# Optimization experiments

Hardware: AMD Instinct MI355X
Metric: run time of the kernel (lower is better)

Reference implementation:

```python
import jax, jax.numpy as jnp
import numpy as np

B = 64; SEQ = 512; PRED = 96; D = 321; HID = 2048
WIN = 64; STRIDE = WIN // 2; FT = WIN // 2 + 1
LOW = int(FT * 0.3); MID = int(FT * 0.4); HIGH = FT - LOW - MID  # 9, 13, 11
NW = SEQ // STRIDE + 1; EMBED = NW * WIN  # 17, 1088
EPS = 1e-5; SCALE = 0.02
LH = int(LOW * 2.0); MH = int(MID * 2.0); HH = int(HIGH * 2.0)  # 18, 26, 22


def _clayer(key, fan_in, fan_out):
    k1, k2, k3, k4 = jax.random.split(key, 4)
    return (jax.random.normal(k1, (fan_in, fan_out), jnp.float32) * SCALE,
            jax.random.normal(k2, (fan_in, fan_out), jnp.float32) * SCALE,
            jax.random.normal(k3, (fan_out,), jnp.float32) * SCALE,
            jax.random.normal(k4, (fan_out,), jnp.float32) * SCALE)


def setup_inputs() -> dict:
    key = jax.random.key(0)
    ks = jax.random.split(key, 12)
    inp = {}
    inp["x"] = jax.random.normal(ks[0], (B, SEQ, D), jnp.float32)
    inp["x_mark_enc"] = jax.random.normal(ks[1], (B, SEQ, 4), jnp.float32)
    inp["x_dec"] = jax.random.normal(ks[2], (B, PRED, D), jnp.float32)
    inp["x_mark_dec"] = jax.random.normal(ks[3], (B, PRED, 4), jnp.float32)
    n = jnp.arange(WIN, dtype=jnp.float32)
    inp["window"] = 0.5 * (1.0 - jnp.cos(2.0 * jnp.pi * n / WIN))  # torch.hann_window (periodic)
    inp["revin_w"] = jnp.ones((D,), jnp.float32)
    inp["revin_b"] = jnp.zeros((D,), jnp.float32)
    # low band filter: 3 complex layers LOW->LH->LH->LOW
    for i, (fi, fo) in enumerate([(LOW, LH), (LH, LH), (LH, LOW)]):
        wr, wi, br, bi = _clayer(jax.random.fold_in(ks[4], i), fi, fo)
        inp[f"low{i}_wr"], inp[f"low{i}_wi"], inp[f"low{i}_br"], inp[f"low{i}_bi"] = wr, wi, br, bi
    # mid band filter: 2 complex layers MID->MH->MID
    for i, (fi, fo) in enumerate([(MID, MH), (MH, MID)]):
        wr, wi, br, bi = _clayer(jax.random.fold_in(ks[5], i), fi, fo)
        inp[f"mid{i}_wr"], inp[f"mid{i}_wi"], inp[f"mid{i}_br"], inp[f"mid{i}_bi"] = wr, wi, br, bi
    # high band filter: 1 complex layer HIGH->HIGH
    wr, wi, br, bi = _clayer(ks[6], HIGH, HIGH)
    inp["high0_wr"], inp["high0_wi"], inp["high0_br"], inp["high0_bi"] = wr, wi, br, bi
    inp["fc1_w"] = jax.random.normal(ks[7], (EMBED, HID), jnp.float32) * SCALE
    inp["fc1_b"] = jnp.zeros((HID,), jnp.float32)
    inp["fc2_w"] = jax.random.normal(ks[8], (HID, PRED), jnp.float32) * SCALE
    inp["fc2_b"] = jnp.zeros((PRED,), jnp.float32)
    return inp


def _clin(z, wr, wi, br, bi):
    return z @ (wr + 1j * wi) + (br + 1j * bi)


def _cact(z):
    return jax.nn.leaky_relu(z.real) + 1j * jax.nn.leaky_relu(z.imag)


def reference(x, x_mark_enc, x_dec, x_mark_dec, window, revin_w, revin_b,
              low0_wr, low0_wi, low0_br, low0_bi,
              low1_wr, low1_wi, low1_br, low1_bi,
              low2_wr, low2_wi, low2_br, low2_bi,
              mid0_wr, mid0_wi, mid0_br, mid0_bi,
              mid1_wr, mid1_wi, mid1_br, mid1_bi,
              high0_wr, high0_wi, high0_br, high0_bi,
              fc1_w, fc1_b, fc2_w, fc2_b):
    # RevIN norm over time dim
    mean = jnp.mean(x, axis=1, keepdims=True)
    std = jnp.sqrt(jnp.var(x, axis=1, keepdims=True) + EPS)
    xn = (x - mean) / std * revin_w + revin_b
    xc = jnp.transpose(xn, (0, 2, 1))                      # [B, D, L]
    xp = jnp.pad(xc, ((0, 0), (0, 0), (STRIDE, STRIDE)))
    # batched window extraction (replaces python loop over windows)
    idx = jnp.arange(NW)[:, None] * STRIDE + jnp.arange(WIN)[None, :]
    seg = xp[:, :, idx]
    w = window / jnp.linalg.norm(window)
    xf = jnp.fft.rfft(seg * w, axis=-1)                    # [B, D, NW, FT] complex
    low = xf[..., :LOW]
    mid = xf[..., LOW:LOW + MID]
    high = xf[..., LOW + MID:]
    low = _clin(_cact(_clin(_cact(_clin(low, low0_wr, low0_wi, low0_br, low0_bi)),
                            low1_wr, low1_wi, low1_br, low1_bi)),
                low2_wr, low2_wi, low2_br, low2_bi)
    mid = _clin(_cact(_clin(mid, mid0_wr, mid0_wi, mid0_br, mid0_bi)),
                mid1_wr, mid1_wi, mid1_br, mid1_bi)
    high = _clin(high, high0_wr, high0_wi, high0_br, high0_bi)
    xfil = jnp.concatenate([low, mid, high], axis=-1)      # [B, D, NW, FT]
    xt = jnp.fft.irfft(xfil, n=WIN, axis=-1)
    emb = xt.reshape(x.shape[0], D, EMBED)
    h = jax.nn.leaky_relu(emb @ fc1_w + fc1_b)
    y = h @ fc2_w + fc2_b                                  # [B, D, PRED]
    y = jnp.transpose(y, (0, 2, 1))                        # [B, PRED, D]
    # RevIN denorm
    y = (y - revin_b) / (revin_w + EPS * EPS) * std + mean
    return y
```

## Files before the change

### kernel.cpp

```cpp
#include <hip/hip_runtime.h>

typedef unsigned short u16;
typedef unsigned int   u32;
typedef __attribute__((ext_vector_type(4))) float  fvec4;
typedef __attribute__((ext_vector_type(8))) __bf16 bvec8;

#define NB    64
#define SEQL  512
#define DCH   321
#define BDTOT (NB * DCH)
#define NWIN  17
#define PREDL 96
#define MWTOT (BDTOT * NWIN)
#define KPAD  1152

__device__ __forceinline__ u16 f2bf(float f) {
    union { float f; u32 u; } v; v.f = f;
    u32 r = v.u + 0x7FFFu + ((v.u >> 16) & 1u);
    return (u16)(r >> 16);
}
__device__ __forceinline__ float lrelu(float v) { return v > 0.f ? v : 0.01f * v; }

__device__ __forceinline__ void gld16(const u16* g, u16* l) {
    __builtin_amdgcn_global_load_lds((const __attribute__((address_space(1))) void*)g,
                                     (__attribute__((address_space(3))) void*)l, 16, 0, 0);
}

__global__ __launch_bounds__(256) void stats_kernel(const float* __restrict__ x,
                                                    float* __restrict__ mean,
                                                    float* __restrict__ rstd,
                                                    float* __restrict__ stdv) {
    __shared__ float ls[2][4][64];
    int i = threadIdx.x & 63;
    int j = threadIdx.x >> 6;
    int bd = blockIdx.x * 64 + i;
    int b = bd / DCH, d = bd - b * DCH;
    float s = 0.f, ss = 0.f;
    for (int t = j; t < SEQL; t += 4) {
        float v = x[((size_t)b * SEQL + t) * DCH + d];
        s += v; ss += v * v;
    }
    ls[0][j][i] = s; ls[1][j][i] = ss;
    __syncthreads();
    if (j == 0) {
        s  = ls[0][0][i] + ls[0][1][i] + ls[0][2][i] + ls[0][3][i];
        ss = ls[1][0][i] + ls[1][1][i] + ls[1][2][i] + ls[1][3][i];
        float m   = s * (1.f / SEQL);
        float var = ss * (1.f / SEQL) - m * m;
        float st  = sqrtf(var + 1e-5f);
        mean[bd] = m; rstd[bd] = 1.f / st; stdv[bd] = st;
    }
}

__global__ __launch_bounds__(256) void norm_transpose(const float* __restrict__ x,
                                                      const float* __restrict__ mean,
                                                      const float* __restrict__ rstd,
                                                      const float* __restrict__ rw,
                                                      const float* __restrict__ rb,
                                                      u16* __restrict__ xnT) {
    __shared__ float tile[64][65];
    int d0 = blockIdx.x * 64, s0 = blockIdx.y * 64, b = blockIdx.z;
    for (int e = threadIdx.x; e < 4096; e += 256) {
        int sr = e >> 6, dc = e & 63;
        int d = d0 + dc;
        tile[sr][dc] = (d < DCH) ? x[((size_t)b * SEQL + s0 + sr) * DCH + d] : 0.f;
    }
    __syncthreads();
    for (int e = threadIdx.x; e < 4096; e += 256) {
        int dr = e >> 6, sc = e & 63;
        int d = d0 + dr;
        if (d < DCH) {
            int bd = b * DCH + d;
            float v = (tile[sc][dr] - mean[bd]) * rstd[bd] * rw[d] + rb[d];
            xnT[(size_t)bd * 576 + 32 + s0 + sc] = f2bf(v);
        }
    }
}

__global__ __launch_bounds__(256) void pad_zero(u16* __restrict__ xnT) {
    int idx = blockIdx.x * 256 + threadIdx.x;
    if (idx < BDTOT * 64) {
        int bd = idx >> 6, q = idx & 63;
        int off = q < 32 ? q : 512 + q;
        xnT[(size_t)bd * 576 + off] = 0;
    }
}

__global__ __launch_bounds__(256) void pad_emb(u16* __restrict__ EMB) {
    int idx = blockIdx.x * 256 + threadIdx.x;
    if (idx < BDTOT * 8) {
        int bd = idx >> 3, o = (idx & 7) * 8;
        fvec4 z = {0.f, 0.f, 0.f, 0.f};
        *(fvec4*)&EMB[(size_t)bd * KPAD + 1088 + o] = z;
    }
}

__global__ __launch_bounds__(256) void precompute_kernel(
    const float* __restrict__ window,
    const float* __restrict__ l0wr, const float* __restrict__ l0wi,
    const float* __restrict__ l0br, const float* __restrict__ l0bi,
    const float* __restrict__ l1wr, const float* __restrict__ l1wi,
    const float* __restrict__ l1br, const float* __restrict__ l1bi,
    const float* __restrict__ l2wr, const float* __restrict__ l2wi,
    const float* __restrict__ l2br, const float* __restrict__ l2bi,
    const float* __restrict__ m0wr, const float* __restrict__ m0wi,
    const float* __restrict__ m0br, const float* __restrict__ m0bi,
    const float* __restrict__ m1wr, const float* __restrict__ m1wi,
    const float* __restrict__ m1br, const float* __restrict__ m1bi,
    const float* __restrict__ h0wr, const float* __restrict__ h0wi,
    const float* __restrict__ h0br, const float* __restrict__ h0bi,
    u16* __restrict__ A1t, u16* __restrict__ W1t, u16* __restrict__ B2t,
    float* __restrict__ bias1, float* __restrict__ bias2, float* __restrict__ biast)
{
    int idx = blockIdx.x * 256 + threadIdx.x;
    float nrm = 0.f;
    for (int i = 0; i < 64; ++i) nrm += window[i] * window[i];
    float inv = 1.0f / sqrtf(nrm);
    const float STEP = 6.283185307179586f / 64.f;
    auto Cc = [&](int n, int k) { return  window[n] * inv * cosf(STEP * (float)((k * n) & 63)); };
    auto Ss = [&](int n, int k) { return -window[n] * inv * sinf(STEP * (float)((k * n) & 63)); };
    auto aRe = [&](int k, int n) {
        float sc = (k == 0 || k == 32) ? (1.f / 64.f) : (2.f / 64.f);
        return sc * cosf(STEP * (float)((k * n) & 63));
    };
    auto aIm = [&](int k, int n) {
        if (k == 0 || k == 32) return 0.f;
        return -(2.f / 64.f) * sinf(STEP * (float)((k * n) & 63));
    };
    if (idx < 16384) {
        int j = idx >> 6, n = idx & 63;
        float v = 0.f;
        if (j < 18)                    { for (int k = 0; k < 9;  ++k) v += Cc(n,k)   *l0wr[k*18+j]      - Ss(n,k)   *l0wi[k*18+j]; }
        else if (j < 36)               { int jj=j-18; for (int k = 0; k < 9;  ++k) v += Cc(n,k)   *l0wi[k*18+jj] + Ss(n,k)   *l0wr[k*18+jj]; }
        else if (j >= 64  && j < 90)   { int jj=j-64; for (int k = 0; k < 13; ++k) v += Cc(n,9+k) *m0wr[k*26+jj] - Ss(n,9+k) *m0wi[k*26+jj]; }
        else if (j >= 90  && j < 116)  { int jj=j-90; for (int k = 0; k < 13; ++k) v += Cc(n,9+k) *m0wi[k*26+jj] + Ss(n,9+k) *m0wr[k*26+jj]; }
        else if (j >= 128 && j < 139)  { int jj=j-128;for (int k = 0; k < 11; ++k) v += Cc(n,22+k)*h0wr[k*11+jj] - Ss(n,22+k)*h0wi[k*11+jj]; }
        else if (j >= 139 && j < 150)  { int jj=j-139;for (int k = 0; k < 11; ++k) v += Cc(n,22+k)*h0wi[k*11+jj] + Ss(n,22+k)*h0wr[k*11+jj]; }
        A1t[idx] = f2bf(v);
    } else if (idx < 24576) {
        int t = idx - 16384; int j = t >> 6, k = t & 63;
        float v = 0.f;
        if (j < 18)      { if (k < 18) v = l1wr[k*18+j];        else if (k < 36) v = -l1wi[(k-18)*18+j]; }
        else if (j < 36) { int jj=j-18; if (k < 18) v = l1wi[k*18+jj]; else if (k < 36) v =  l1wr[(k-18)*18+jj]; }
        W1t[t] = f2bf(v);
    } else if (idx < 49152) {
        int t = idx - 24576; int n = t / 192, c = t - n * 192;
        float v = 0.f;
        if (n < 64) {
            if (c < 18)                  { for (int m = 0; m < 9;  ++m) v +=  l2wr[c*9+m]     *aRe(m,n)   + l2wi[c*9+m]     *aIm(m,n); }
            else if (c < 36)             { int cc=c-18; for (int m = 0; m < 9;  ++m) v += -l2wi[cc*9+m]   *aRe(m,n)   + l2wr[cc*9+m]   *aIm(m,n); }
            else if (c >= 64 && c < 90)  { int cc=c-64; for (int m = 0; m < 13; ++m) v +=  m1wr[cc*13+m]  *aRe(9+m,n) + m1wi[cc*13+m]  *aIm(9+m,n); }
            else if (c >= 90 && c < 116) { int cc=c-90; for (int m = 0; m < 13; ++m) v += -m1wi[cc*13+m]  *aRe(9+m,n) + m1wr[cc*13+m]  *aIm(9+m,n); }
            else if (c >= 128 && c < 139){ v = aRe(22 + (c-128), n); }
            else if (c >= 139 && c < 150){ v = aIm(22 + (c-139), n); }
        }
        B2t[t] = f2bf(v);
    } else if (idx < 49344) {
        int c = idx - 49152;
        float v = 0.f;
        if (c < 18) v = l0br[c];
        else if (c < 36) v = l0bi[c-18];
        else if (c >= 64 && c < 90) v = m0br[c-64];
        else if (c >= 90 && c < 116) v = m0bi[c-90];
        bias1[c] = v;
    } else if (idx < 49472) {
        int c = idx - 49344;
        float v = 0.f;
        if (c < 18) v = l1br[c]; else if (c < 36) v = l1bi[c-18];
        bias2[c] = v;
    } else if (idx < 49536) {
        int n = idx - 49472;
        float v = 0.f;
        for (int k = 0; k <= 32; ++k) {
            float br = (k < 9) ? l2br[k] : (k < 22 ? m1br[k-9] : h0br[k-22]);
            float bi = (k < 9) ? l2bi[k] : (k < 22 ? m1bi[k-9] : h0bi[k-22]);
            v += aRe(k, n) * br + aIm(k, n) * bi;
        }
        biast[n] = v;
    }
}

__global__ __launch_bounds__(256) void wtrans(const float* __restrict__ W, u16* __restrict__ Wt,
                                              int R, int C, int Cpad, int ldw) {
    __shared__ float t[32][33];
    int c0 = blockIdx.x * 32, r0 = blockIdx.y * 32;
    for (int e = threadIdx.x; e < 1024; e += 256) {
        int rr = e >> 5, cc = e & 31;
        int rg = r0 + rr, cg = c0 + cc;
        t[rr][cc] = (rg < R && cg < C) ? W[(size_t)rg * C + cg] : 0.f;
    }
    __syncthreads();
    for (int e = threadIdx.x; e < 1024; e += 256) {
        int cr = e >> 5, rc = e & 31;
        int cg = c0 + cr, rg = r0 + rc;
        if (cg < Cpad && rg < ldw) Wt[(size_t)cg * ldw + rg] = f2bf(t[rc][cr]);
    }
}

__global__ __launch_bounds__(256) void spectral_fused(
    const u16* __restrict__ xnT, const u16* __restrict__ A1t,
    const u16* __restrict__ W1t, const u16* __restrict__ B2t,
    const float* __restrict__ bias1, const float* __restrict__ bias2,
    const float* __restrict__ biast, u16* __restrict__ EMB)
{
    __shared__ u16 XB[64 * 72];
    __shared__ u16 ACT[64 * 208];
    const int tid  = threadIdx.x;
    const int lane = tid & 63;
    const int wn   = tid >> 6;
    const int r0   = blockIdx.x * 64;

    {
        int rr = tid >> 2;
        int cc = (tid & 3) * 16;
        u32 gr = (u32)(r0 + rr);
        u32 bd = gr / 17u, nw = gr - bd * 17u;
        const u16* src = xnT + (size_t)bd * 576 + nw * 32 + cc;
        *(bvec8*)&XB[rr * 72 + cc]     = *(const bvec8*)(src);
        *(bvec8*)&XB[rr * 72 + cc + 8] = *(const bvec8*)(src + 8);
    }
    __syncthreads();

    fvec4 acc1[4][3] = {};
#pragma unroll
    for (int kk = 0; kk < 2; ++kk) {
        int ko = kk * 32 + ((lane >> 4) << 3);
        bvec8 af[4], bf[3];
#pragma unroll
        for (int m = 0; m < 4; ++m)
            af[m] = *(const bvec8*)&XB[(m * 16 + (lane & 15)) * 72 + ko];
#pragma unroll
        for (int n = 0; n < 3; ++n)
            bf[n] = *(const bvec8*)(A1t + (size_t)(wn * 48 + n * 16 + (lane & 15)) * 64 + ko);
#pragma unroll
        for (int m = 0; m < 4; ++m)
#pragma unroll
            for (int n = 0; n < 3; ++n)
                acc1[m][n] = __builtin_amdgcn_mfma_f32_16x16x32_bf16(af[m], bf[n], acc1[m][n], 0, 0, 0);
    }
#pragma unroll
    for (int n = 0; n < 3; ++n) {
        int col = wn * 48 + n * 16 + (lane & 15);
        float bs = bias1[col];
#pragma unroll
        for (int m = 0; m < 4; ++m)
#pragma unroll
            for (int q = 0; q < 4; ++q) {
                int row = m * 16 + ((lane >> 4) << 2) + q;
                float v = acc1[m][n][q] + bs;
                if (col < 128) v = lrelu(v);
                ACT[row * 208 + col] = f2bf(v);
            }
    }
    __syncthreads();

    fvec4 acc2[4] = {};
#pragma unroll
    for (int kk = 0; kk < 2; ++kk) {
        int ko = kk * 32 + ((lane >> 4) << 3);
        bvec8 bf = *(const bvec8*)(W1t + (size_t)(wn * 16 + (lane & 15)) * 64 + ko);
#pragma unroll
        for (int m = 0; m < 4; ++m) {
            bvec8 af = *(const bvec8*)&ACT[(m * 16 + (lane & 15)) * 208 + ko];
            acc2[m] = __builtin_amdgcn_mfma_f32_16x16x32_bf16(af, bf, acc2[m], 0, 0, 0);
        }
    }
    __syncthreads();
    {
        int col = wn * 16 + (lane & 15);
        float bs = bias2[col];
#pragma unroll
        for (int m = 0; m < 4; ++m)
#pragma unroll
            for (int q = 0; q < 4; ++q) {
                int row = m * 16 + ((lane >> 4) << 2) + q;
                ACT[row * 208 + col] = f2bf(lrelu(acc2[m][q] + bs));
            }
    }
    __syncthreads();

    fvec4 acc3[4] = {};
#pragma unroll
    for (int kk = 0; kk < 6; ++kk) {
        int ko = kk * 32 + ((lane >> 4) << 3);
        bvec8 bf = *(const bvec8*)(B2t + (size_t)(wn * 16 + (lane & 15)) * 192 + ko);
#pragma unroll
        for (int m = 0; m < 4; ++m) {
            bvec8 af = *(const bvec8*)&ACT[(m * 16 + (lane & 15)) * 208 + ko];
            acc3[m] = __builtin_amdgcn_mfma_f32_16x16x32_bf16(af, bf, acc3[m], 0, 0, 0);
        }
    }
    {
        int col = wn * 16 + (lane & 15);
        float bs = biast[col];
#pragma unroll
        for (int m = 0; m < 4; ++m)
#pragma unroll
            for (int q = 0; q < 4; ++q) {
                int row = m * 16 + ((lane >> 4) << 2) + q;
                int wr = r0 + row;
                int bd2 = wr / 17, nw2 = wr - bd2 * 17;
                EMB[(size_t)bd2 * KPAD + nw2 * 64 + col] = f2bf(acc3[m][q] + bs);
            }
    }
}

template <int SWZ>
__global__ __launch_bounds__(512, 2) void gemm256_8ph(
    const u16* __restrict__ A, const u16* __restrict__ Bt,
    const float* __restrict__ bias, u16* __restrict__ C,
    int Mloc, int K, int ldc, long long a_off, int nwg)
{
    extern __shared__ u16 lds[];
    const int tid  = threadIdx.x;
    const int lane = tid & 63;
    const int l15  = lane & 15;
    const int hi   = lane >> 4;
    const int wid  = tid >> 6;
    const int wm   = wid >> 2;
    const int wn   = wid & 3;
    int wg;
    if (SWZ) {
        int bid = blockIdx.x;
        int q = nwg >> 3, r = nwg & 7, xcd = bid & 7, off = bid >> 3;
        wg = (xcd < r) ? (xcd * (q + 1) + off) : (r * (q + 1) + (xcd - r) * q + off);
    } else wg = blockIdx.x;
    const int mt = wg >> 3;
    const int nt = wg & 7;
    const int bm0 = mt * 256, bn0 = nt * 256;

    const u16* sbase[4][2];
#pragma unroll
    for (int u = 0; u < 4; ++u) {
        const int mat = u >> 1, half = u & 1;
#pragma unroll
        for (int j = 0; j < 2; ++j) {
            int idx = j * 512 + tid;
            int row = half * 128 + (idx >> 3);
            int kc = ((idx & 7) ^ (row & 7)) << 3;
            if (mat == 0) {
                int rl = bm0 + row; if (rl > Mloc - 1) rl = Mloc - 1;
                sbase[u][j] = A + (size_t)(a_off + rl) * K + kc;
            } else {
                sbase[u][j] = Bt + (size_t)(bn0 + row) * K + kc;
            }
        }
    }
    auto stage_unit = [&](int bufb, int tg, int u) {
        const int mat = u >> 1, half = u & 1;
        u16* dstb = lds + bufb * 32768 + mat * 16384 + half * 8192;
#pragma unroll
        for (int j = 0; j < 2; ++j) {
            int idx = j * 512 + tid;
            gld16(sbase[u][j] + ((size_t)tg << 6), dstb + idx * 8);
        }
    };

    fvec4 acc[8][4] = {};
    const int NT = K >> 6;

#pragma unroll
    for (int u = 0; u < 4; ++u) stage_unit(0, 0, u);
    asm volatile("s_waitcnt vmcnt(0)" ::: "memory");
    __builtin_amdgcn_sched_barrier(0);
    __builtin_amdgcn_s_barrier();
    __builtin_amdgcn_sched_barrier(0);

    for (int t = 0; t < NT; ++t) {
        const int cur = t & 1;
        const u16* Ab = lds + cur * 32768;
        const u16* Bb = Ab + 16384;
        const bool notlast = (t < NT - 1);
        bvec8 bfr[4];
#pragma unroll
        for (int p = 0; p < 4; ++p) {
            const int kk = p >> 1, mh = p & 1;
            bvec8 af[4];
            if (mh == 0) {
#pragma unroll
                for (int n = 0; n < 4; ++n) {
                    int r = wn * 64 + n * 16 + l15;
                    int bc = (kk * 4 + hi) ^ (l15 & 7);
                    bfr[n] = *(const bvec8*)&Bb[r * 64 + bc * 8];
                }
            }
#pragma unroll
            for (int mm = 0; mm < 4; ++mm) {
                int r = wm * 128 + (mh * 4 + mm) * 16 + l15;
                int bc = (kk * 4 + hi) ^ (l15 & 7);
                af[mm] = *(const bvec8*)&Ab[r * 64 + bc * 8];
            }
            if (notlast) stage_unit(cur ^ 1, t + 1, p);
            __builtin_amdgcn_sched_barrier(0);
            __builtin_amdgcn_s_barrier();
            __builtin_amdgcn_sched_barrier(0);
            __builtin_amdgcn_s_setprio(1);
#pragma unroll
            for (int mm = 0; mm < 4; ++mm)
#pragma unroll
                for (int n = 0; n < 4; ++n)
                    acc[mh * 4 + mm][n] = __builtin_amdgcn_mfma_f32_16x16x32_bf16(
                        af[mm], bfr[n], acc[mh * 4 + mm][n], 0, 0, 0);
            __builtin_amdgcn_s_setprio(0);
            if (p == 3) {
                asm volatile("s_waitcnt vmcnt(0)" ::: "memory");
            }
            __builtin_amdgcn_sched_barrier(0);
            __builtin_amdgcn_s_barrier();
            __builtin_amdgcn_sched_barrier(0);
        }
    }

#pragma unroll
    for (int m = 0; m < 8; ++m) {
        int rl0 = bm0 + wm * 128 + m * 16 + ((lane >> 4) << 2);
#pragma unroll
        for (int n = 0; n < 4; ++n) {
            int col = bn0 + wn * 64 + n * 16 + l15;
            float bs = bias[col];
#pragma unroll
            for (int q = 0; q < 4; ++q) {
                int rl = rl0 + q;
                if (rl < Mloc)
                    C[(size_t)rl * (size_t)ldc + col] = f2bf(lrelu(acc[m][n][q] + bs));
            }
        }
    }
}

__global__ __launch_bounds__(256) void gemm_bt_splitk(
    const u16* __restrict__ A, const u16* __restrict__ Bt,
    void* __restrict__ Cp, int Mloc, int N, int K, int lda, int ldc,
    long long c_off, int klen, long long pstride)
{
    const int tid  = threadIdx.x;
    const int lane = tid & 63;
    const int wm   = (tid >> 7) & 1;
    const int wn   = (tid >> 6) & 1;
    const int mt = blockIdx.y;
    int k0 = blockIdx.x * klen;
    int k1 = (k0 + klen > K) ? K : k0 + klen;
    const int bn0 = 0;
    const int bm0 = mt * 128;
    __shared__ u16 Als[128 * 64];
    __shared__ u16 Bls[128 * 64];
    fvec4 acc[4][4] = {};

    for (int kt = k0; kt < k1; kt += 64) {
#pragma unroll
        for (int i = 0; i < 4; ++i) {
            int idx = i * 256 + tid;
            int r  = idx >> 3;
            int kc = (idx & 7) << 3;
            int rl = bm0 + r; if (rl > Mloc - 1) rl = Mloc - 1;
            gld16(A + (size_t)rl * lda + kt + kc, &Als[idx * 8]);
            gld16(Bt + (size_t)(bn0 + r) * K + kt + kc, &Bls[idx * 8]);
        }
        __syncthreads();
#pragma unroll
        for (int kk = 0; kk < 2; ++kk) {
            int ko = kk * 32 + ((lane >> 4) << 3);
            bvec8 af[4], bfr[4];
#pragma unroll
            for (int m = 0; m < 4; ++m)
                af[m] = *(const bvec8*)&Als[(wm * 64 + m * 16 + (lane & 15)) * 64 + ko];
#pragma unroll
            for (int n = 0; n < 4; ++n)
                bfr[n] = *(const bvec8*)&Bls[(wn * 64 + n * 16 + (lane & 15)) * 64 + ko];
#pragma unroll
            for (int m = 0; m < 4; ++m)
#pragma unroll
                for (int n = 0; n < 4; ++n)
                    acc[m][n] = __builtin_amdgcn_mfma_f32_16x16x32_bf16(af[m], bfr[n], acc[m][n], 0, 0, 0);
        }
        __syncthreads();
    }

#pragma unroll
    for (int m = 0; m < 4; ++m) {
        int rbase = bm0 + wm * 64 + m * 16 + ((lane >> 4) << 2);
#pragma unroll
        for (int n = 0; n < 4; ++n) {
            int col = bn0 + wn * 64 + n * 16 + (lane & 15);
            if (col < N) {
#pragma unroll
                for (int q = 0; q < 4; ++q) {
                    int rl = rbase + q;
                    if (rl < Mloc) {
                        float* yp = (float*)Cp + (size_t)blockIdx.x * pstride;
                        yp[(size_t)(c_off + rl) * ldc + col] = acc[m][n][q];
                    }
                }
            }
        }
    }
}

__global__ __launch_bounds__(256) void final_denorm(const float* __restrict__ YP,
                                                    const float* __restrict__ fc2b,
                                                    const float* __restrict__ mean,
                                                    const float* __restrict__ stdv,
                                                    const float* __restrict__ rw,
                                                    const float* __restrict__ rb,
                                                    float* __restrict__ out) {
    const long long PART = (long long)BDTOT * PREDL;
    __shared__ float t[32][33];
    int d0 = blockIdx.x * 32, p0 = blockIdx.y * 32, b = blockIdx.z;
    for (int e = threadIdx.x; e < 1024; e += 256) {
        int di = e >> 5, pj = e & 31;
        int d = d0 + di, p = p0 + pj;
        if (d < DCH && p < PREDL) {
            size_t off = ((size_t)b * DCH + d) * PREDL + p;
            t[di][pj] = YP[off] + YP[off + PART] + YP[off + 2 * PART] + fc2b[p];
        } else t[di][pj] = 0.f;
    }
    __syncthreads();
    for (int e = threadIdx.x; e < 1024; e += 256) {
        int pi = e >> 5, dj = e & 31;
        int d = d0 + dj, p = p0 + pi;
        if (d < DCH && p < PREDL) {
            int bd = b * DCH + d;
            float v = (t[dj][pi] - rb[d]) / (rw[d] + 1e-10f) * stdv[bd] + mean[bd];
            out[((size_t)b * PREDL + p) * DCH + d] = v;
        }
    }
}

extern "C" void kernel_launch(void* const* d_in, const int* in_sizes, int n_in,
                              void* d_out, int out_size, void* d_ws, size_t ws_size,
                              hipStream_t stream) {
    const float* x      = (const float*)d_in[0];
    const float* window = (const float*)d_in[4];
    const float* rw     = (const float*)d_in[5];
    const float* rb     = (const float*)d_in[6];
    const float* l0wr = (const float*)d_in[7],  *l0wi = (const float*)d_in[8];
    const float* l0br = (const float*)d_in[9],  *l0bi = (const float*)d_in[10];
    const float* l1wr = (const float*)d_in[11], *l1wi = (const float*)d_in[12];
    const float* l1br = (const float*)d_in[13], *l1bi = (const float*)d_in[14];
    const float* l2wr = (const float*)d_in[15], *l2wi = (const float*)d_in[16];
    const float* l2br = (const float*)d_in[17], *l2bi = (const float*)d_in[18];
    const float* m0wr = (const float*)d_in[19], *m0wi = (const float*)d_in[20];
    const float* m0br = (const float*)d_in[21], *m0bi = (const float*)d_in[22];
    const float* m1wr = (const float*)d_in[23], *m1wi = (const float*)d_in[24];
    const float* m1br = (const float*)d_in[25], *m1bi = (const float*)d_in[26];
    const float* h0wr = (const float*)d_in[27], *h0wi = (const float*)d_in[28];
    const float* h0br = (const float*)d_in[29], *h0bi = (const float*)d_in[30];
    const float* fc1w = (const float*)d_in[31];
    const float* fc1b = (const float*)d_in[32];
    const float* fc2w = (const float*)d_in[33];
    const float* fc2b = (const float*)d_in[34];

    char* p = (char*)d_ws;
    auto alloc = [&](size_t n) { char* r = p; p += (n + 255) & ~(size_t)255; return r; };
    float* mean  = (float*)alloc(BDTOT * 4);
    float* rstd  = (float*)alloc(BDTOT * 4);
    float* stdv  = (float*)alloc(BDTOT * 4);
    float* bias1 = (float*)alloc(192 * 4);
    float* bias2 = (float*)alloc(128 * 4);
    float* biast = (float*)alloc(64 * 4);
    u16* A1t   = (u16*)alloc(256 * 64 * 2);
    u16* W1t   = (u16*)alloc(128 * 64 * 2);
    u16* B2t   = (u16*)alloc(128 * 192 * 2);
    u16* fc1wT = (u16*)alloc((size_t)2048 * KPAD * 2);
    u16* fc2wT = (u16*)alloc((size_t)128 * 2048 * 2);
    u16* xnT   = (u16*)alloc((size_t)BDTOT * 576 * 2);
    float* YP  = (float*)xnT;
    u16* EMB   = (u16*)alloc((size_t)BDTOT * KPAD * 2);

    size_t fixed_end = (size_t)(p - (char*)d_ws);
    int CH = 16;
    const int chs[5] = {1, 2, 4, 8, 16};
    for (int ci = 0; ci < 5; ++ci) {
        int c = chs[ci];
        size_t hbuf = (size_t)(BDTOT / c) * 2048 * 2;
        if (fixed_end + hbuf <= ws_size) { CH = c; break; }
    }
    int bd_c = BDTOT / CH;
    u16* Hbuf = (u16*)p;

    hipFuncSetAttribute(reinterpret_cast<const void*>(&gemm256_8ph<1>),
                        hipFuncAttributeMaxDynamicSharedMemorySize, 131072);

    dim3 blk(256);
    stats_kernel<<<BDTOT / 64, blk, 0, stream>>>(x, mean, rstd, stdv);
    norm_transpose<<<dim3(6, 8, NB), blk, 0, stream>>>(x, mean, rstd, rw, rb, xnT);
    pad_zero<<<(BDTOT * 64 + 255) / 256, blk, 0, stream>>>(xnT);
    precompute_kernel<<<194, blk, 0, stream>>>(window,
        l0wr, l0wi, l0br, l0bi, l1wr, l1wi, l1br, l1bi, l2wr, l2wi, l2br, l2bi,
        m0wr, m0wi, m0br, m0bi, m1wr, m1wi, m1br, m1bi, h0wr, h0wi, h0br, h0bi,
        A1t, W1t, B2t, bias1, bias2, biast);
    wtrans<<<dim3(64, 36), blk, 0, stream>>>(fc1w, fc1wT, 1088, 2048, 2048, KPAD);
    wtrans<<<dim3(4, 64),  blk, 0, stream>>>(fc2w, fc2wT, 2048, 96, 128, 2048);

    spectral_fused<<<MWTOT / 64, blk, 0, stream>>>(xnT, A1t, W1t, B2t, bias1, bias2, biast, EMB);
    pad_emb<<<(BDTOT * 8 + 255) / 256, blk, 0, stream>>>(EMB);

    const long long PART = (long long)BDTOT * PREDL;
    for (int c = 0; c < CH; ++c) {
        long long boff = (long long)c * bd_c;
        int gm = (bd_c + 255) / 256;
        int nwg = 8 * gm;
        gemm256_8ph<1><<<dim3(nwg), dim3(512), 131072, stream>>>(EMB, fc1wT, fc1b, Hbuf,
            bd_c, KPAD, 2048, boff, nwg);
        gemm_bt_splitk<<<dim3(3, (bd_c + 127) / 128), blk, 0, stream>>>(Hbuf, fc2wT, YP,
            bd_c, 96, 2048, 2048, 96, boff, 704, PART);
    }
    final_denorm<<<dim3(11, 3, NB), blk, 0, stream>>>(YP, fc2b, mean, stdv, rw, rb, (float*)d_out);
}
```

Measured before the change: 321.3 us.

## Reorder fc1 GEMM staging by k-half and use partial vmcnt waits

The fc1 GEMM's shared-memory layout is reorganized so each staging unit loads a half of A rows or a k-half of B. Loads can then complete in phase order, and the single full vmcnt(0) wait at the end of each k-tile becomes partial waits spread across phases. The aim is to overlap global-to-LDS loads with MFMA work for longer instead of draining all loads at once. B tiles use a new 32-element-wide swizzle, which risks different LDS bank-conflict behaviour and subtle correctness bugs in the wait counts.

```diff
diff --git a/kernel.cpp b/kernel.cpp
--- a/kernel.cpp
+++ b/kernel.cpp
@@ -306,7 +306,7 @@
 }
 
 template <int SWZ>
-__global__ __launch_bounds__(512, 2) void gemm256_8ph(
+__global__ __launch_bounds__(512, 2) void gemm256_cv(
     const u16* __restrict__ A, const u16* __restrict__ Bt,
     const float* __restrict__ bias, u16* __restrict__ C,
     int Mloc, int K, int ldc, long long a_off, int nwg)
@@ -332,23 +332,24 @@
     const u16* sbase[4][2];
 #pragma unroll
     for (int u = 0; u < 4; ++u) {
-        const int mat = u >> 1, half = u & 1;
 #pragma unroll
         for (int j = 0; j < 2; ++j) {
             int idx = j * 512 + tid;
-            int row = half * 128 + (idx >> 3);
-            int kc = ((idx & 7) ^ (row & 7)) << 3;
-            if (mat == 0) {
+            if ((u & 1) == 0) {
+                int row = (u >> 1) * 128 + (idx >> 3);
+                int kc = ((idx & 7) ^ (row & 7)) << 3;
                 int rl = bm0 + row; if (rl > Mloc - 1) rl = Mloc - 1;
                 sbase[u][j] = A + (size_t)(a_off + rl) * K + kc;
             } else {
+                int row = idx >> 2;
+                int kc = (u >> 1) * 32 + (((idx & 3) ^ ((row >> 1) & 3)) << 3);
                 sbase[u][j] = Bt + (size_t)(bn0 + row) * K + kc;
             }
         }
     }
     auto stage_unit = [&](int bufb, int tg, int u) {
-        const int mat = u >> 1, half = u & 1;
-        u16* dstb = lds + bufb * 32768 + mat * 16384 + half * 8192;
+        int base = ((u & 1) == 0) ? ((u >> 1) * 8192) : (16384 + (u >> 1) * 8192);
+        u16* dstb = lds + bufb * 32768 + base;
 #pragma unroll
         for (int j = 0; j < 2; ++j) {
             int idx = j * 512 + tid;
@@ -380,15 +381,15 @@
 #pragma unroll
                 for (int n = 0; n < 4; ++n) {
                     int r = wn * 64 + n * 16 + l15;
-                    int bc = (kk * 4 + hi) ^ (l15 & 7);
-                    bfr[n] = *(const bvec8*)&Bb[r * 64 + bc * 8];
+                    int ch = hi ^ ((r >> 1) & 3);
+                    bfr[n] = *(const bvec8*)&Bb[kk * 8192 + r * 32 + ch * 8];
                 }
             }
 #pragma unroll
             for (int mm = 0; mm < 4; ++mm) {
                 int r = wm * 128 + (mh * 4 + mm) * 16 + l15;
-                int bc = (kk * 4 + hi) ^ (l15 & 7);
-                af[mm] = *(const bvec8*)&Ab[r * 64 + bc * 8];
+                int ch = (kk * 4 + hi) ^ (r & 7);
+                af[mm] = *(const bvec8*)&Ab[r * 64 + ch * 8];
             }
             if (notlast) stage_unit(cur ^ 1, t + 1, p);
             __builtin_amdgcn_sched_barrier(0);
@@ -402,8 +403,14 @@
                     acc[mh * 4 + mm][n] = __builtin_amdgcn_mfma_f32_16x16x32_bf16(
                         af[mm], bfr[n], acc[mh * 4 + mm][n], 0, 0, 0);
             __builtin_amdgcn_s_setprio(0);
-            if (p == 3) {
-                asm volatile("s_waitcnt vmcnt(0)" ::: "memory");
+            if (p == 0) {
+                if (notlast) asm volatile("s_waitcnt vmcnt(4)" ::: "memory");
+                else         asm volatile("s_waitcnt vmcnt(2)" ::: "memory");
+            } else if (p == 1) {
+                if (notlast) asm volatile("s_waitcnt vmcnt(4)" ::: "memory");
+                else         asm volatile("s_waitcnt vmcnt(0)" ::: "memory");
+            } else if (p == 3) {
+                if (notlast) asm volatile("s_waitcnt vmcnt(4)" ::: "memory");
             }
             __builtin_amdgcn_sched_barrier(0);
             __builtin_amdgcn_s_barrier();
@@ -578,7 +585,7 @@
     int bd_c = BDTOT / CH;
     u16* Hbuf = (u16*)p;
 
-    hipFuncSetAttribute(reinterpret_cast<const void*>(&gemm256_8ph<1>),
+    hipFuncSetAttribute(reinterpret_cast<const void*>(&gemm256_cv<1>),
                         hipFuncAttributeMaxDynamicSharedMemorySize, 131072);
 
     dim3 blk(256);
@@ -600,7 +607,7 @@
         long long boff = (long long)c * bd_c;
         int gm = (bd_c + 255) / 256;
         int nwg = 8 * gm;
-        gemm256_8ph<1><<<dim3(nwg), dim3(512), 131072, stream>>>(EMB, fc1wT, fc1b, Hbuf,
+        gemm256_cv<1><<<dim3(nwg), dim3(512), 131072, stream>>>(EMB, fc1wT, fc1b, Hbuf,
             bd_c, KPAD, 2048, boff, nwg);
         gemm_bt_splitk<<<dim3(3, (bd_c + 127) / 128), blk, 0, stream>>>(Hbuf, fc2wT, YP,
             bd_c, 96, 2048, 2048, 96, boff, 704, PART);
```

Result: no change. 321.5 us (+0.1%).
